# Optimization experiments

Measured on AMD Instinct MI355X. Metric: run time of the kernel, lower is better.

## Reference

```python
import jax, jax.numpy as jnp
import numpy as np

B, K, T, C, F = 2048, 32, 365, 4, 128  # batch, prototypes, steps, bands, feature_size


def conv1d(x, w, b, pad):
    # x: (B, Cin, T), w: (Cout, Cin, Kw)
    y = jax.lax.conv_general_dilated(x, w, (1,), [(pad, pad)],
                                     dimension_numbers=('NCH', 'OIH', 'NCH'))
    return y + b[None, :, None]


def bn_relu(x, gamma, beta):
    # training-mode BatchNorm1d over (batch, time) per channel
    mu = x.mean((0, 2), keepdims=True)
    var = x.var((0, 2), keepdims=True)
    xn = (x - mu) * jax.lax.rsqrt(var + 1e-5)
    return jax.nn.relu(xn * gamma[None, :, None] + beta[None, :, None])


def encoder(x, w1, b1, g1, be1, w2, b2, g2, be2, w3, b3, g3, be3, fc_w, fc_b):
    # FCNBaseline: 3 conv blocks + global average pool + linear
    h = x.transpose(0, 2, 1)                    # (B, C, T)
    h = bn_relu(conv1d(h, w1, b1, 4), g1, be1)  # (B, 128, T+1)
    h = bn_relu(conv1d(h, w2, b2, 2), g2, be2)  # (B, 256, *)
    h = bn_relu(conv1d(h, w3, b3, 1), g3, be3)  # (B, 128, *)
    return h.mean(-1) @ fc_w.T + fc_b           # (B, F)


def setup_inputs() -> dict:
    key = jax.random.key(0)
    ks = jax.random.split(key, 12)
    input_seq = jax.random.normal(ks[0], (B, T, C), jnp.float32)
    label = jax.random.randint(ks[1], (B,), 0, 9)
    mask = (jax.random.uniform(ks[2], (B, T)) > 0.2).astype(jnp.float32)
    prototypes = jax.random.normal(ks[3], (K, T, C), jnp.float32)
    w1 = jax.random.normal(ks[4], (128, C, 8)) * 0.05
    b1 = jnp.zeros((128,)); g1 = jnp.ones((128,)); be1 = jnp.zeros((128,))
    w2 = jax.random.normal(ks[5], (256, 128, 5)) * 0.05
    b2 = jnp.zeros((256,)); g2 = jnp.ones((256,)); be2 = jnp.zeros((256,))
    w3 = jax.random.normal(ks[6], (128, 256, 3)) * 0.05
    b3 = jnp.zeros((128,)); g3 = jnp.ones((128,)); be3 = jnp.zeros((128,))
    fc_w = jax.random.normal(ks[7], (F, 128)) * 0.05
    fc_b = jnp.zeros((F,))
    off_w = jax.random.normal(ks[8], (K * C, F)) * 0.05
    off_b = jnp.zeros((K * C,))
    return dict(input_seq=input_seq, label=label, mask=mask, prototypes=prototypes,
                w1=w1, b1=b1, g1=g1, be1=be1, w2=w2, b2=b2, g2=g2, be2=be2,
                w3=w3, b3=b3, g3=g3, be3=be3, fc_w=fc_w, fc_b=fc_b,
                off_w=off_w, off_b=off_b)


def reference(input_seq, label, mask, prototypes, w1, b1, g1, be1, w2, b2, g2, be2,
              w3, b3, g3, be3, fc_w, fc_b, off_w, off_b):
    # trans_activ=False (TPS warp disabled), offset_activ=True, unsupervised path
    feat = encoder(input_seq, w1, b1, g1, be1, w2, b2, g2, be2, w3, b3, g3, be3, fc_w, fc_b)
    offset = jnp.tanh(feat @ off_w.T + off_b).reshape(-1, K, 1, C)  # (B,K,1,C)
    protos = prototypes[None] + offset                              # (B,K,T,C)
    diff = input_seq[:, None] - protos                              # (B,K,T,C)
    # masked squared-distance reduce: mask (B,T) broadcasts over (K,C)
    distances = jnp.einsum('bktc,bt->bk', diff * diff, mask)        # (B,K)
    indices = jnp.argmin(distances, axis=1)                         # (B,)
    output_seq = jnp.take_along_axis(protos, indices[:, None, None, None], axis=1)[:, 0]
    return output_seq
```

## Files before the change

### kernel.cpp

```cpp
#include <hip/hip_runtime.h>
#include <hip/hip_bf16.h>

#define BB 2048
#define TIN 365
#define TO 366
#define C1 128
#define C2 256
#define C3 128
#define FF 128

typedef __attribute__((ext_vector_type(4))) float f32x4v;
typedef __attribute__((ext_vector_type(8))) short bf16x8;

__device__ inline unsigned short f2bf(float v) {
  unsigned u = __float_as_uint(v);
  unsigned r = (u + 0x7FFF + ((u >> 16) & 1)) >> 16;
  return (unsigned short)r;
}
__device__ inline float bf2f(unsigned short b) {
  return __uint_as_float(((unsigned)b) << 16);
}

__global__ void wtrans_kernel(const float* __restrict__ wsrc, float* __restrict__ wdst,
                              int Cout, int Cin, int Kw) {
// ... 21 lines not shown
    size_t dst = ((((size_t)k * 4 + (i >> 5)) * 16 + (o >> 4)) * 64 +
                  ((i >> 3) & 3) * 16 + (o & 15)) * 8 + (i & 7);
    wh[dst] = (short)hb;
    wl[dst] = (short)lb;
  }
}
__global__ void wprep3_kernel(const float* __restrict__ w3,
                              short* __restrict__ wh, short* __restrict__ wl) {
  int n = 128 * 256 * 3;
  for (int idx = blockIdx.x * 256 + threadIdx.x; idx < n; idx += gridDim.x * 256) {
    int k = idx % 3;
    int rest = idx / 3;
    int i = rest % 256;
    int o = rest / 256;
    float v = w3[idx];
    unsigned short hb = f2bf(v);
    unsigned short lb = f2bf(v - bf2f(hb));
    size_t dst = ((((size_t)k * 8 + (i >> 5)) * 8 + (o >> 4)) * 64 +
                  ((i >> 3) & 3) * 16 + (o & 15)) * 8 + (i & 7);
    wh[dst] = (short)hb;
    wl[dst] = (short)lb;
  }
}

__global__ void bnparam_kernel(const double* __restrict__ sums,
                               const float* __restrict__ gamma,
                               const float* __restrict__ beta, int Cch,
                               float* __restrict__ scale, float* __restrict__ shift) {
  int i = threadIdx.x;
  if (i < Cch) {
    const double N = (double)BB * (double)TO;
    double mean = sums[i] / N;
    double var = sums[Cch + i] / N - mean * mean;
    double sc = (double)gamma[i] / sqrt(var + 1e-5);
    scale[i] = (float)sc;
    shift[i] = (float)((double)beta[i] - mean * sc);
  }
}

__global__ __launch_bounds__(256) void conv1_stats_kernel(
    const float* __restrict__ x, const float* __restrict__ w1,
    const float* __restrict__ b1, double* __restrict__ sums) {
  __shared__ float4 xs[374];
  __shared__ float ws1[4096];
  int tid = threadIdx.x;
  for (int i = tid; i < 4096; i += 256) ws1[i] = w1[i];
  __syncthreads();
  const int o = tid >> 1, half = tid & 1;
  float wr[32];
#pragma unroll
  for (int i = 0; i < 32; ++i) wr[i] = ws1[o * 32 + i];
  const float bo = b1[o];
  float s1 = 0.f, s2 = 0.f;
  for (int b = blockIdx.x * 8; b < blockIdx.x * 8 + 8; ++b) {
    __syncthreads();
    for (int u = tid; u < 374; u += 256) {
      int t_in = u - 4;
      float4 v = make_float4(0.f, 0.f, 0.f, 0.f);
      if (t_in >= 0 && t_in < TIN) v = *(const float4*)(x + ((size_t)b * TIN + t_in) * 4);
      xs[u] = v;
    }
    __syncthreads();
    for (int t = half * 183; t < half * 183 + 183; ++t) {
      float acc = bo;
#pragma unroll
      for (int k = 0; k < 8; ++k) {
        float4 xv = xs[t + k];
        acc = fmaf(wr[k], xv.x, acc);
        acc = fmaf(wr[8 + k], xv.y, acc);
        acc = fmaf(wr[16 + k], xv.z, acc);
        acc = fmaf(wr[24 + k], xv.w, acc);
      }
      s1 += acc; s2 += acc * acc;
    }
  }
  s1 += __shfl_xor(s1, 1);
  s2 += __shfl_xor(s2, 1);
  if (half == 0) {
    atomicAdd(&sums[o], (double)s1);
    atomicAdd(&sums[C1 + o], (double)s2);
  }
}

__global__ __launch_bounds__(256) void conv2_mfma_kernel(
    const float* __restrict__ x, const float* __restrict__ w1g,
    const float* __restrict__ b1, const float* __restrict__ scale1,
    const float* __restrict__ shift1, const short* __restrict__ w2ph,
    const short* __restrict__ w2pl, const float* __restrict__ b2,
    float* __restrict__ p2) {
  __shared__ float ws1[4096];
  __shared__ float4 xwin[76];
  __shared__ __align__(16) short h1h[68 * 72];
  __shared__ __align__(16) short h1l[68 * 72];
  __shared__ float sstat[512];
  const int tid = threadIdx.x;
  const int tt = blockIdx.x, b = blockIdx.y;
  const int tbase = tt * 64;
  const int slice = (b * 6 + tt) & 63;
  const int w = tid >> 6, lane = tid & 63;
  const int q = lane >> 4, l15 = lane & 15;

  for (int i = tid; i < 4096; i += 256) ws1[i] = w1g[i];
  for (int u = tid; u < 76; u += 256) {
    int tx = tbase - 6 + u;
    float4 v = make_float4(0.f, 0.f, 0.f, 0.f);
    if (tx >= 0 && tx < TIN) v = *(const float4*)(x + ((size_t)b * TIN + tx) * 4);
    xwin[u] = v;
  }
  float b2r[4][4];
#pragma unroll
  for (int om = 0; om < 4; ++om)
#pragma unroll
    for (int r = 0; r < 4; ++r) b2r[om][r] = b2[64 * w + om * 16 + q * 4 + r];

  f32x4v acc[4][4];
#pragma unroll
  for (int om = 0; om < 4; ++om)
#pragma unroll
    for (int nt = 0; nt < 4; ++nt) acc[om][nt] = (f32x4v){0.f, 0.f, 0.f, 0.f};

  const int chl = tid >> 2, qt = tid & 3;
  for (int ic2 = 0; ic2 < 2; ++ic2) {
    __syncthreads();
    {
      int ch = ic2 * 64 + chl;
      float sc = scale1[ch], sh = shift1[ch], bo = b1[ch];
      const float* wr = &ws1[ch * 32];
      for (int j = 0; j < 17; ++j) {
        int u = qt * 17 + j;
        int t = tbase - 2 + u;
        float a = bo;
#pragma unroll
        for (int kk = 0; kk < 8; ++kk) {
          float4 xv = xwin[u + kk];
          a = fmaf(wr[kk], xv.x, a);
          a = fmaf(wr[8 + kk], xv.y, a);
          a = fmaf(wr[16 + kk], xv.z, a);
          a = fmaf(wr[24 + kk], xv.w, a);
        }
        float v = (t >= 0 && t < TO) ? fmaxf(fmaf(sc, a, sh), 0.f) : 0.f;
        unsigned short hb = f2bf(v);
        h1h[u * 72 + chl] = (short)hb;
        h1l[u * 72 + chl] = (short)f2bf(v - bf2f(hb));
      }
    }
    __syncthreads();
    for (int k = 0; k < 5; ++k) {
      for (int ic = 0; ic < 2; ++ic) {
        int icg = ic2 * 2 + ic;
        bf16x8 ah[4], al[4];
#pragma unroll
        for (int om = 0; om < 4; ++om) {
          int og = 4 * w + om;
          size_t base = ((((size_t)k * 4 + icg) * 16 + og) * 64 + lane) * 8;
          ah[om] = *(const bf16x8*)(w2ph + base);
          al[om] = *(const bf16x8*)(w2pl + base);
        }
        int ioff = ic * 32 + q * 8;
#pragma unroll
        for (int nt = 0; nt < 4; ++nt) {
          int u = nt * 16 + l15 + k;
          bf16x8 bh = *(const bf16x8*)&h1h[u * 72 + ioff];
          bf16x8 bl = *(const bf16x8*)&h1l[u * 72 + ioff];
#pragma unroll
          for (int om = 0; om < 4; ++om) {
            acc[om][nt] = __builtin_amdgcn_mfma_f32_16x16x32_bf16(ah[om], bh, acc[om][nt], 0, 0, 0);
            acc[om][nt] = __builtin_amdgcn_mfma_f32_16x16x32_bf16(ah[om], bl, acc[om][nt], 0, 0, 0);
            acc[om][nt] = __builtin_amdgcn_mfma_f32_16x16x32_bf16(al[om], bh, acc[om][nt], 0, 0, 0);
          }
        }
      }
    }
  }
  float ts1[16], ts2[16];
#pragma unroll
  for (int i = 0; i < 16; ++i) { ts1[i] = 0.f; ts2[i] = 0.f; }
#pragma unroll
  for (int om = 0; om < 4; ++om)
#pragma unroll
    for (int nt = 0; nt < 4; ++nt) {
      int t = tbase + nt * 16 + l15;
      if (t < TO) {
#pragma unroll
        for (int r = 0; r < 4; ++r) {
          float v = acc[om][nt][r] + b2r[om][r];
          ts1[om * 4 + r] += v;
          ts2[om * 4 + r] += v * v;
        }
      }
    }
#pragma unroll
  for (int i = 0; i < 16; ++i) {
#pragma unroll
    for (int d = 1; d < 16; d <<= 1) {
      ts1[i] += __shfl_xor(ts1[i], d);
      ts2[i] += __shfl_xor(ts2[i], d);
    }
  }
  if (l15 == 0) {
#pragma unroll
    for (int om = 0; om < 4; ++om)
#pragma unroll
      for (int r = 0; r < 4; ++r) {
        int o = 64 * w + om * 16 + q * 4 + r;
        sstat[o] = ts1[om * 4 + r];
        sstat[256 + o] = ts2[om * 4 + r];
      }
  }
  __syncthreads();
  atomicAdd(&p2[(size_t)tid * 64 + slice], sstat[tid]);
  atomicAdd(&p2[((size_t)tid + 256) * 64 + slice], sstat[tid + 256]);
}

template <int EPI>
__global__ __launch_bounds__(256) void fused23_kernel(
    const float* __restrict__ x, const float* __restrict__ w1g,
    const float* __restrict__ b1, const float* __restrict__ scale1,
    const float* __restrict__ shift1, const short* __restrict__ w2ph,
    const short* __restrict__ w2pl, const float* __restrict__ b2,
    const float* __restrict__ scale2, const float* __restrict__ shift2,
    const short* __restrict__ w3ph, const short* __restrict__ w3pl,
    const float* __restrict__ b3, const float* __restrict__ scale3,
    const float* __restrict__ shift3, float* __restrict__ p3,
    float* __restrict__ pooled) {
  __shared__ float4 xwin[80];
  __shared__ __align__(16) short un[34848];
  __shared__ float bn2s[768];
  __shared__ float sstat[256];
  short* h1h = un;
  short* h1l = un + 70 * 72;
  short* h2sh = un;
  short* h2sl = un + 66 * 264;
  const int tid = threadIdx.x;
  const int tt = blockIdx.x, b = blockIdx.y;
  const int tbase = tt * 64;
  const int slice = (b * 6 + tt) & 63;
  const int w = tid >> 6, lane = tid & 63;
  const int q = lane >> 4, l15 = lane & 15;

  for (int u = tid; u < 77; u += 256) {
    int tx = tbase - 7 + u;
    float4 v = make_float4(0.f, 0.f, 0.f, 0.f);
    if (tx >= 0 && tx < TIN) v = *(const float4*)(x + ((size_t)b * TIN + tx) * 4);
    xwin[u] = v;
  }
  bn2s[tid] = b2[tid];
  bn2s[256 + tid] = scale2[tid];
  bn2s[512 + tid] = shift2[tid];

  float b3r[2][4], sc3r[2][4], sh3r[2][4];
#pragma unroll
  for (int om = 0; om < 2; ++om)
#pragma unroll
    for (int r = 0; r < 4; ++r) {
      int o = 32 * w + om * 16 + q * 4 + r;
      b3r[om][r] = b3[o];
      if (EPI == 1) { sc3r[om][r] = scale3[o]; sh3r[om][r] = shift3[o]; }
    }

  f32x4v acc2[4][5];
#pragma unroll
  for (int om = 0; om < 4; ++om)
#pragma unroll
    for (int nt = 0; nt < 5; ++nt) acc2[om][nt] = (f32x4v){0.f, 0.f, 0.f, 0.f};

  const int chl = tid >> 2, qt = tid & 3;
  for (int ic2 = 0; ic2 < 2; ++ic2) {
    int ch = ic2 * 64 + chl;
    float wr[32];
#pragma unroll
    for (int i = 0; i < 32; ++i) wr[i] = w1g[ch * 32 + i];
    float sc = scale1[ch], sh = shift1[ch], bo = b1[ch];
    __syncthreads();
    for (int j = 0; j < 18; ++j) {
      int u1 = qt * 18 + j;
      if (u1 < 70) {
        int t1 = tbase - 3 + u1;
        float a = bo;
#pragma unroll
        for (int kk = 0; kk < 8; ++kk) {
          float4 xv = xwin[u1 + kk];
          a = fmaf(wr[kk], xv.x, a);
          a = fmaf(wr[8 + kk], xv.y, a);
          a = fmaf(wr[16 + kk], xv.z, a);
          a = fmaf(wr[24 + kk], xv.w, a);
        }
        float v = (t1 >= 0 && t1 < TO) ? fmaxf(fmaf(sc, a, sh), 0.f) : 0.f;
        unsigned short hb = f2bf(v);
        h1h[u1 * 72 + chl] = (short)hb;
        h1l[u1 * 72 + chl] = (short)f2bf(v - bf2f(hb));
      }
    }
    __syncthreads();
    for (int k = 0; k < 5; ++k) {
// ... 81 lines not shown
      }
    }
  }
  if (EPI == 0) {
    float ts1[8], ts2[8];
#pragma unroll
    for (int i = 0; i < 8; ++i) { ts1[i] = 0.f; ts2[i] = 0.f; }
#pragma unroll
    for (int om = 0; om < 2; ++om)
#pragma unroll
      for (int nt = 0; nt < 4; ++nt) {
        int t = tbase + nt * 16 + l15;
        if (t < TO) {
#pragma unroll
          for (int r = 0; r < 4; ++r) {
            float v = acc3[om][nt][r] + b3r[om][r];
            ts1[om * 4 + r] += v;
            ts2[om * 4 + r] += v * v;
          }
        }
      }
#pragma unroll
    for (int i = 0; i < 8; ++i) {
#pragma unroll
      for (int d = 1; d < 16; d <<= 1) {
        ts1[i] += __shfl_xor(ts1[i], d);
        ts2[i] += __shfl_xor(ts2[i], d);
      }
    }
    if (l15 == 0) {
#pragma unroll
      for (int om = 0; om < 2; ++om)
#pragma unroll
        for (int r = 0; r < 4; ++r) {
          int o = 32 * w + om * 16 + q * 4 + r;
          sstat[o] = ts1[om * 4 + r];
          sstat[128 + o] = ts2[om * 4 + r];
        }
    }
    __syncthreads();
    atomicAdd(&p3[(size_t)tid * 64 + slice], sstat[tid]);
  } else {
    float ps[8];
#pragma unroll
    for (int i = 0; i < 8; ++i) ps[i] = 0.f;
#pragma unroll
    for (int om = 0; om < 2; ++om)
#pragma unroll
      for (int nt = 0; nt < 4; ++nt) {
        int t = tbase + nt * 16 + l15;
        if (t < TO) {
#pragma unroll
          for (int r = 0; r < 4; ++r) {
            float v = acc3[om][nt][r] + b3r[om][r];
            ps[om * 4 + r] += fmaxf(fmaf(sc3r[om][r], v, sh3r[om][r]), 0.f);
          }
        }
      }
#pragma unroll
    for (int i = 0; i < 8; ++i) {
#pragma unroll
      for (int d = 1; d < 16; d <<= 1) ps[i] += __shfl_xor(ps[i], d);
    }
    if (l15 == 0) {
#pragma unroll
      for (int om = 0; om < 2; ++om)
#pragma unroll
        for (int r = 0; r < 4; ++r) {
          int o = 32 * w + om * 16 + q * 4 + r;
          atomicAdd(&pooled[(size_t)b * 128 + o], ps[om * 4 + r]);
        }
    }
  }
}

__global__ __launch_bounds__(64) void reduce_slices_kernel(
    const float* __restrict__ p, double* __restrict__ sums) {
  int c = blockIdx.x, tid = threadIdx.x;
  double s = (double)p[(size_t)c * 64 + tid];
  for (int d = 32; d > 0; d >>= 1) s += __shfl_down(s, d);
  if (tid == 0) sums[c] = s;
}

__global__ __launch_bounds__(256) void conv12_kernel(
    const float* __restrict__ x, const float* __restrict__ w1g,
    const float* __restrict__ b1, const float* __restrict__ scale1,
    const float* __restrict__ shift1, const float* __restrict__ w2t,
    const float* __restrict__ b2, double* __restrict__ sums2) {
  __shared__ __align__(16) float xs[32][72];
  __shared__ __align__(16) float wsb[32 * 5 * 64];
  __shared__ float4 xwin[80];
  __shared__ float ws1[4096];
  __shared__ float s1s[64], s2s[64];
  const int tid = threadIdx.x;
  const int tbase = blockIdx.x * 64;
  const int obase = blockIdx.y * 64;
  const int bb0 = blockIdx.z * 16;
  for (int i = tid; i < 4096; i += 256) ws1[i] = w1g[i];
  if (tid < 64) { s1s[tid] = 0.f; s2s[tid] = 0.f; }
  const int t0 = (tid & 15) * 4;
  const int o0 = (tid >> 4) * 4;
  const int mch = tid >> 3, mug = tid & 7;
  float b2r[4];
#pragma unroll
  for (int oo = 0; oo < 4; ++oo) b2r[oo] = b2[obase + o0 + oo];
  float ts1[4] = {}, ts2[4] = {};
  for (int b = bb0; b < bb0 + 16; ++b) {
    __syncthreads();
    for (int u = tid; u < 76; u += 256) {
      int tx = tbase - 6 + u;
      float4 v = make_float4(0.f, 0.f, 0.f, 0.f);
      if (tx >= 0 && tx < TIN) v = *(const float4*)(x + ((size_t)b * TIN + tx) * 4);
      xwin[u] = v;
    }
    __syncthreads();
    float acc[4][4] = {};
    for (int ic = 0; ic < C1; ic += 32) {
      {
        int ch = ic + mch;
        float wr[32];
#pragma unroll
        for (int i = 0; i < 32; ++i) wr[i] = ws1[ch * 32 + i];
        float bo = b1[ch], sc = scale1[ch], sh = shift1[ch];
#pragma unroll
        for (int j = 0; j < 9; ++j) {
          int uu = mug * 9 + j;
          if (uu < 68) {
            int v = tbase - 2 + uu;
            float a = bo;
#pragma unroll
            for (int k = 0; k < 8; ++k) {
              float4 xv = xwin[uu + k];
              a = fmaf(wr[k], xv.x, a);
              a = fmaf(wr[8 + k], xv.y, a);
              a = fmaf(wr[16 + k], xv.z, a);
              a = fmaf(wr[24 + k], xv.w, a);
            }
            xs[mch][uu] = (v >= 0 && v < TO) ? fmaxf(fmaf(sc, a, sh), 0.f) : 0.f;
          }
        }
      }
      {
        const float* wsrc = w2t + (size_t)(ic * 5) * C2 + obase;
        for (int idx = tid; idx < 32 * 5 * 64; idx += 256) {
          int o = idx & 63, row = idx >> 6;
          wsb[idx] = wsrc[(size_t)row * C2 + o];
        }
      }
      __syncthreads();
#pragma unroll 4
      for (int ii = 0; ii < 32; ++ii) {
        float xv[8];
#pragma unroll
        for (int d = 0; d < 8; ++d) xv[d] = xs[ii][t0 + d];
#pragma unroll
        for (int k = 0; k < 5; ++k) {
          float4 wv = *(const float4*)&wsb[(ii * 5 + k) * 64 + o0];
#pragma unroll
          for (int tz = 0; tz < 4; ++tz) {
            float xvv = xv[k + tz];
            acc[0][tz] = fmaf(wv.x, xvv, acc[0][tz]);
            acc[1][tz] = fmaf(wv.y, xvv, acc[1][tz]);
            acc[2][tz] = fmaf(wv.z, xvv, acc[2][tz]);
            acc[3][tz] = fmaf(wv.w, xvv, acc[3][tz]);
          }
        }
      }
      __syncthreads();
    }
#pragma unroll
    for (int oo = 0; oo < 4; ++oo) {
#pragma unroll
      for (int tz = 0; tz < 4; ++tz) {
        int t = tbase + t0 + tz;
        if (t < TO) {
          float v = acc[oo][tz] + b2r[oo];
          ts1[oo] += v; ts2[oo] += v * v;
        }
      }
    }
  }
  __syncthreads();
#pragma unroll
  for (int oo = 0; oo < 4; ++oo) {
    atomicAdd(&s1s[o0 + oo], ts1[oo]);
    atomicAdd(&s2s[o0 + oo], ts2[oo]);
  }
  __syncthreads();
  if (tid < 64) {
    atomicAdd(&sums2[obase + tid], (double)s1s[tid]);
    atomicAdd(&sums2[C2 + obase + tid], (double)s2s[tid]);
  }
}

template <int EPI>
__global__ __launch_bounds__(256) void conv23_kernel(
    const float* __restrict__ x, const float* __restrict__ w1g,
    const float* __restrict__ b1, const float* __restrict__ scale1,
    const float* __restrict__ shift1, const float* __restrict__ w2t,
    const float* __restrict__ b2, const float* __restrict__ scale2,
    const float* __restrict__ shift2, const float* __restrict__ w3t,
    const float* __restrict__ b3, const float* __restrict__ scale3,
    const float* __restrict__ shift3, double* __restrict__ sums3,
    float* __restrict__ pooled) {
  __shared__ float4 xwin[80];
  __shared__ float ws1[4096];
  __shared__ float h1buf[128][72];
  __shared__ float h2c[32][68];
  __shared__ float red[128], red2[128];
  const int tid = threadIdx.x;
  const int tbase = blockIdx.x * 64;
  const int bb0 = blockIdx.y * 8;
  for (int i = tid; i < 4096; i += 256) ws1[i] = w1g[i];
  const int t3 = (tid & 15) * 4;
  const int og = tid >> 4;
  float b3r[8], sc3r[8], sh3r[8];
#pragma unroll
  for (int oo = 0; oo < 8; ++oo) {
    int o = og * 8 + oo;
    b3r[oo] = b3[o];
    if (EPI == 1) { sc3r[oo] = scale3[o]; sh3r[oo] = shift3[o]; }
  }
  const int c1ch = tid >> 1, c1half = tid & 1;
  float wr1[32]; float c1b = 0.f, c1sc = 0.f, c1sh = 0.f;
  const int oc2 = tid & 31, ug = tid >> 5;
  const int base2 = ug * 9;
  const int jmax = (66 - base2) < 9 ? (66 - base2) : 9;
  float ts1[8] = {}, ts2[8] = {};
  bool wr1_loaded = false;
  for (int b = bb0; b < bb0 + 8; ++b) {
    __syncthreads();
    for (int u = tid; u < 78; u += 256) {
      int tx = tbase - 7 + u;
      float4 v = make_float4(0.f, 0.f, 0.f, 0.f);
      if (tx >= 0 && tx < TIN) v = *(const float4*)(x + ((size_t)b * TIN + tx) * 4);
      xwin[u] = v;
    }
    __syncthreads();
    if (!wr1_loaded) {
#pragma unroll
      for (int i = 0; i < 32; ++i) wr1[i] = ws1[c1ch * 32 + i];
      c1b = b1[c1ch]; c1sc = scale1[c1ch]; c1sh = shift1[c1ch];
      wr1_loaded = true;
    }
    for (int j = 0; j < 35; ++j) {
      int uu = c1half * 35 + j;
      int v = tbase - 3 + uu;
      float a = c1b;
#pragma unroll
      for (int k = 0; k < 8; ++k) {
        float4 xv = xwin[uu + k];
        a = fmaf(wr1[k], xv.x, a);
        a = fmaf(wr1[8 + k], xv.y, a);
        a = fmaf(wr1[16 + k], xv.z, a);
        a = fmaf(wr1[24 + k], xv.w, a);
      }
      h1buf[c1ch][uu] = (v >= 0 && v < TO) ? fmaxf(fmaf(c1sc, a, c1sh), 0.f) : 0.f;
    }
    float acc3[8][4] = {};
    for (int ocb = 0; ocb < 8; ++ocb) {
      __syncthreads();
      {
        int oc = ocb * 32 + oc2;
        float acc2[9];
#pragma unroll
        for (int j = 0; j < 9; ++j) acc2[j] = 0.f;
        for (int i = 0; i < 128; ++i) {
          const float* wrow = w2t + (size_t)i * 5 * C2 + oc;
          float wk0 = wrow[0], wk1 = wrow[C2], wk2 = wrow[2 * C2],
                wk3 = wrow[3 * C2], wk4 = wrow[4 * C2];
          float w0 = h1buf[i][base2 + 0], w1v = h1buf[i][base2 + 1],
                w2v = h1buf[i][base2 + 2], w3v = h1buf[i][base2 + 3],
                w4v = h1buf[i][base2 + 4];
#pragma unroll
          for (int j = 0; j < 9; ++j) {
            if (j < jmax) {
              float s = wk0 * w0;
              s = fmaf(wk1, w1v, s);
              s = fmaf(wk2, w2v, s);
              s = fmaf(wk3, w3v, s);
              s = fmaf(wk4, w4v, s);
              acc2[j] += s;
              if (j + 1 < jmax) {
                w0 = w1v; w1v = w2v; w2v = w3v; w3v = w4v;
                w4v = h1buf[i][base2 + j + 5];
              }
            }
          }
        }
        float bo2 = b2[oc], sc2v = scale2[oc], sh2v = shift2[oc];
#pragma unroll
        for (int j = 0; j < 9; ++j) {
          if (j < jmax) {
            int uu = base2 + j;
            int u = tbase - 1 + uu;
            float v = acc2[j] + bo2;
            h2c[oc2][uu] = (u >= 0 && u < TO) ? fmaxf(fmaf(sc2v, v, sh2v), 0.f) : 0.f;
          }
        }
      }
      __syncthreads();
      for (int i2 = 0; i2 < 32; ++i2) {
        int i = ocb * 32 + i2;
        float h0 = h2c[i2][t3 + 0], h1v = h2c[i2][t3 + 1], h2v = h2c[i2][t3 + 2],
              h3v = h2c[i2][t3 + 3], h4v = h2c[i2][t3 + 4], h5v = h2c[i2][t3 + 5];
        const float* w3row = w3t + (size_t)i * 3 * C3 + og * 8;
#pragma unroll
        for (int k = 0; k < 3; ++k) {
          float4 wa = *(const float4*)(w3row + k * C3);
          float4 wb = *(const float4*)(w3row + k * C3 + 4);
          float hv0 = (k == 0) ? h0 : ((k == 1) ? h1v : h2v);
          float hv1 = (k == 0) ? h1v : ((k == 1) ? h2v : h3v);
          float hv2 = (k == 0) ? h2v : ((k == 1) ? h3v : h4v);
          float hv3 = (k == 0) ? h3v : ((k == 1) ? h4v : h5v);
          float hv[4] = {hv0, hv1, hv2, hv3};
#pragma unroll
          for (int tz = 0; tz < 4; ++tz) {
            acc3[0][tz] = fmaf(wa.x, hv[tz], acc3[0][tz]);
            acc3[1][tz] = fmaf(wa.y, hv[tz], acc3[1][tz]);
            acc3[2][tz] = fmaf(wa.z, hv[tz], acc3[2][tz]);
            acc3[3][tz] = fmaf(wa.w, hv[tz], acc3[3][tz]);
            acc3[4][tz] = fmaf(wb.x, hv[tz], acc3[4][tz]);
            acc3[5][tz] = fmaf(wb.y, hv[tz], acc3[5][tz]);
            acc3[6][tz] = fmaf(wb.z, hv[tz], acc3[6][tz]);
            acc3[7][tz] = fmaf(wb.w, hv[tz], acc3[7][tz]);
          }
        }
      }
    }
    if (EPI == 0) {
#pragma unroll
      for (int oo = 0; oo < 8; ++oo) {
#pragma unroll
        for (int tz = 0; tz < 4; ++tz) {
          int t = tbase + t3 + tz;
          if (t < TO) {
            float v = acc3[oo][tz] + b3r[oo];
            ts1[oo] += v; ts2[oo] += v * v;
          }
        }
      }
    } else {
      __syncthreads();
      if (tid < 128) red[tid] = 0.f;
      __syncthreads();
#pragma unroll
      for (int oo = 0; oo < 8; ++oo) {
        float s = 0.f;
#pragma unroll
        for (int tz = 0; tz < 4; ++tz) {
          int t = tbase + t3 + tz;
          if (t < TO)
            s += fmaxf(fmaf(sc3r[oo], acc3[oo][tz] + b3r[oo], sh3r[oo]), 0.f);
        }
        atomicAdd(&red[og * 8 + oo], s);
      }
      __syncthreads();
      if (tid < 128) atomicAdd(&pooled[(size_t)b * C3 + tid], red[tid]);
    }
  }
  if (EPI == 0) {
    __syncthreads();
    if (tid < 128) { red[tid] = 0.f; red2[tid] = 0.f; }
    __syncthreads();
#pragma unroll
    for (int oo = 0; oo < 8; ++oo) {
      atomicAdd(&red[og * 8 + oo], ts1[oo]);
      atomicAdd(&red2[og * 8 + oo], ts2[oo]);
    }
    __syncthreads();
    if (tid < 128) {
      atomicAdd(&sums3[tid], (double)red[tid]);
      atomicAdd(&sums3[C3 + tid], (double)red2[tid]);
    }
  }
}

__global__ __launch_bounds__(128) void head2_kernel(
    const float* __restrict__ pooled, const float* __restrict__ fc_w,
    const float* __restrict__ fc_b, const float* __restrict__ off_w,
    const float* __restrict__ off_b, float* __restrict__ offs) {
  int b = blockIdx.x, tid = threadIdx.x;
  __shared__ float pl[128], feat[128];
  pl[tid] = pooled[(size_t)b * C3 + tid] * (1.0f / 366.0f);
  __syncthreads();
  {
    const float* wr = fc_w + tid * FF;
    float a = fc_b[tid];
    for (int i = 0; i < 128; ++i) a = fmaf(pl[i], wr[i], a);
    feat[tid] = a;
  }
  __syncthreads();
  {
    const float* wr = off_w + tid * FF;
    float z = off_b[tid];
    for (int i = 0; i < 128; ++i) z = fmaf(feat[i], wr[i], z);
    offs[(size_t)b * 128 + tid] = tanhf(z);
  }
}

__global__ __launch_bounds__(256) void dist_kernel(
    const float* __restrict__ x, const float* __restrict__ mask,
    const float* __restrict__ protos, const float* __restrict__ offs,
    float* __restrict__ out) {
  int b = blockIdx.x, tid = threadIdx.x;
  __shared__ float ofl[128];
  __shared__ double dred[256];
  __shared__ int ksel;
  if (tid < 128) ofl[tid] = offs[(size_t)b * 128 + tid];
  __syncthreads();
  int k = tid & 31, tg = tid >> 5;
  float o0 = ofl[k * 4 + 0], o1 = ofl[k * 4 + 1], o2 = ofl[k * 4 + 2], o3 = ofl[k * 4 + 3];
  double acc = 0.0;
  for (int t = tg; t < TIN; t += 8) {
    float4 xv = *(const float4*)(x + ((size_t)b * TIN + t) * 4);
    float4 pv = *(const float4*)(protos + ((size_t)k * TIN + t) * 4);
    float m = mask[(size_t)b * TIN + t];
    float d0 = xv.x - pv.x - o0;
    float d1 = xv.y - pv.y - o1;
    float d2 = xv.z - pv.z - o2;
    float d3 = xv.w - pv.w - o3;
    acc += (double)(m * (d0 * d0 + d1 * d1 + d2 * d2 + d3 * d3));
  }
  dred[tid] = acc;
  __syncthreads();
  if (tid < 32) {
    double s = 0.0;
    for (int g = 0; g < 8; ++g) s += dred[g * 32 + tid];
    dred[tid] = s;
  }
  __syncthreads();
  if (tid == 0) {
    double best = dred[0]; int bi = 0;
    for (int kk = 1; kk < 32; ++kk)
      if (dred[kk] < best) { best = dred[kk]; bi = kk; }
    ksel = bi;
  }
  __syncthreads();
  int km = ksel;
  const float* psrc = protos + (size_t)km * TIN * 4;
  float* dst = out + (size_t)b * TIN * 4;
  for (int u = tid; u < TIN * 4; u += 256)
    dst[u] = psrc[u] + ofl[km * 4 + (u & 3)];
}

extern "C" void kernel_launch(void* const* d_in, const int* in_sizes, int n_in,
                              void* d_out, int out_size, void* d_ws, size_t ws_size,
                              hipStream_t stream) {
  const float* x      = (const float*)d_in[0];
  const float* mask   = (const float*)d_in[2];
  const float* protos = (const float*)d_in[3];
  const float* w1 = (const float*)d_in[4];
  const float* b1 = (const float*)d_in[5];
  const float* g1 = (const float*)d_in[6];
  const float* be1 = (const float*)d_in[7];
  const float* w2 = (const float*)d_in[8];
  const float* b2 = (const float*)d_in[9];
  const float* g2 = (const float*)d_in[10];
  const float* be2 = (const float*)d_in[11];
  const float* w3 = (const float*)d_in[12];
  const float* b3 = (const float*)d_in[13];
  const float* g3 = (const float*)d_in[14];
  const float* be3 = (const float*)d_in[15];
  const float* fc_w = (const float*)d_in[16];
  const float* fc_b = (const float*)d_in[17];
  const float* off_w = (const float*)d_in[18];
  const float* off_b = (const float*)d_in[19];
  float* out = (float*)d_out;
  (void)in_sizes; (void)n_in; (void)out_size;

  char* wsp = (char*)d_ws;
  size_t off = 0;
  auto alloc = [&](size_t bytes) { void* p = wsp + off; off += (bytes + 255) & ~(size_t)255; return p; };
  float* w2t   = (float*)alloc((size_t)C1 * 5 * C2 * 4);
  float* w3t   = (float*)alloc((size_t)C2 * 3 * C3 * 4);
  float* bnp   = (float*)alloc(1024 * 4);
  float* offs  = (float*)alloc((size_t)BB * 128 * 4);
  size_t zero_beg = off;
  double* sums  = (double*)alloc(1024 * 8);
  float* pooled = (float*)alloc((size_t)BB * C3 * 4);
  float* p2     = (float*)alloc((size_t)512 * 64 * 4);
  float* p3     = (float*)alloc((size_t)256 * 64 * 4);
  size_t zero_end = off;
  short* w2ph = (short*)alloc((size_t)256 * 128 * 5 * 2);
  short* w2pl = (short*)alloc((size_t)256 * 128 * 5 * 2);
  short* w3ph = (short*)alloc((size_t)128 * 256 * 3 * 2);
  short* w3pl = (short*)alloc((size_t)128 * 256 * 3 * 2);
  size_t small_end = off;
  const bool mfma_ok = ws_size >= small_end;

  double* sums1 = sums;
  double* sums2 = sums + 256;
  double* sums3 = sums + 768;
  float* scale1 = bnp;        float* shift1 = bnp + 128;
  float* scale2 = bnp + 256;  float* shift2 = bnp + 512;
  float* scale3 = bnp + 768;  float* shift3 = bnp + 896;

  hipMemsetAsync(wsp + zero_beg, 0, zero_end - zero_beg, stream);

  conv1_stats_kernel<<<256, 256, 0, stream>>>(x, w1, b1, sums1);
  bnparam_kernel<<<1, 256, 0, stream>>>(sums1, g1, be1, C1, scale1, shift1);

  if (mfma_ok) {
    wprep2_kernel<<<256, 256, 0, stream>>>(w2, w2ph, w2pl);
    wprep3_kernel<<<128, 256, 0, stream>>>(w3, w3ph, w3pl);

    conv2_mfma_kernel<<<dim3(6, BB), 256, 0, stream>>>(
        x, w1, b1, scale1, shift1, w2ph, w2pl, b2, p2);
    reduce_slices_kernel<<<512, 64, 0, stream>>>(p2, sums2);
    bnparam_kernel<<<1, 256, 0, stream>>>(sums2, g2, be2, C2, scale2, shift2);

    fused23_kernel<0><<<dim3(6, BB), 256, 0, stream>>>(
        x, w1, b1, scale1, shift1, w2ph, w2pl, b2, scale2, shift2,
        w3ph, w3pl, b3, scale3, shift3, p3, pooled);
    reduce_slices_kernel<<<256, 64, 0, stream>>>(p3, sums3);
    bnparam_kernel<<<1, 256, 0, stream>>>(sums3, g3, be3, C3, scale3, shift3);

    fused23_kernel<1><<<dim3(6, BB), 256, 0, stream>>>(
        x, w1, b1, scale1, shift1, w2ph, w2pl, b2, scale2, shift2,
        w3ph, w3pl, b3, scale3, shift3, p3, pooled);
  } else {
    wtrans_kernel<<<256, 256, 0, stream>>>(w2, w2t, C2, C1, 5);
    wtrans_kernel<<<96, 256, 0, stream>>>(w3, w3t, C3, C2, 3);
    conv12_kernel<<<dim3(6, 4, 128), 256, 0, stream>>>(
        x, w1, b1, scale1, shift1, w2t, b2, sums2);
    bnparam_kernel<<<1, 256, 0, stream>>>(sums2, g2, be2, C2, scale2, shift2);
    conv23_kernel<0><<<dim3(6, 256), 256, 0, stream>>>(
        x, w1, b1, scale1, shift1, w2t, b2, scale2, shift2, w3t, b3, scale3, shift3,
        sums3, pooled);
    bnparam_kernel<<<1, 256, 0, stream>>>(sums3, g3, be3, C3, scale3, shift3);
    conv23_kernel<1><<<dim3(6, 256), 256, 0, stream>>>(
        x, w1, b1, scale1, shift1, w2t, b2, scale2, shift2, w3t, b3, scale3, shift3,
        sums3, pooled);
  }

  head2_kernel<<<BB, 128, 0, stream>>>(pooled, fc_w, fc_b, off_w, off_b, offs);
  dist_kernel<<<BB, 256, 0, stream>>>(x, mask, protos, offs, out);
}
```

Baseline: 3.879 ms.

## Materialize conv2 output in workspace instead of recomputing conv1+conv2 per pass

The conv2 MFMA pass now also stores its pre-BN output to a large global buffer. Two new conv3-only passes read that buffer, apply BN2+ReLU, split to bf16 hi/lo and run the conv3 MFMA. The old fused kernels recomputed conv1 and conv2 in both conv3 passes. This trades heavy recomputation for roughly 770MB of writes plus two reads of it. The new path only runs when the workspace is large enough, and the scalar fallback kernels are removed.

```diff
diff --git a/kernel.cpp b/kernel.cpp
--- a/kernel.cpp
+++ b/kernel.cpp
@@ -127,12 +127,13 @@
   }
 }
 
+template <bool STORE>
 __global__ __launch_bounds__(256) void conv2_mfma_kernel(
     const float* __restrict__ x, const float* __restrict__ w1g,
     const float* __restrict__ b1, const float* __restrict__ scale1,
     const float* __restrict__ shift1, const short* __restrict__ w2ph,
     const short* __restrict__ w2pl, const float* __restrict__ b2,
-    float* __restrict__ p2) {
+    float* __restrict__ p2, float* __restrict__ h2g) {
   __shared__ float ws1[4096];
   __shared__ float4 xwin[76];
   __shared__ __align__(16) short h1h[68 * 72];
@@ -231,6 +232,10 @@
           float v = acc[om][nt][r] + b2r[om][r];
           ts1[om * 4 + r] += v;
           ts2[om * 4 + r] += v * v;
+          if (STORE) {
+            int o = 64 * w + om * 16 + q * 4 + r;
+            h2g[((size_t)b * 256 + o) * 368 + t] = v;
+          }
         }
       }
     }
@@ -255,6 +260,156 @@
   __syncthreads();
   atomicAdd(&p2[(size_t)tid * 64 + slice], sstat[tid]);
   atomicAdd(&p2[((size_t)tid + 256) * 64 + slice], sstat[tid + 256]);
+}
+
+template <int EPI>
+__global__ __launch_bounds__(256) void conv3_pass_kernel(
+    const float* __restrict__ h2g, const float* __restrict__ scale2,
+    const float* __restrict__ shift2, const short* __restrict__ w3ph,
+    const short* __restrict__ w3pl, const float* __restrict__ b3,
+    const float* __restrict__ scale3, const float* __restrict__ shift3,
+    float* __restrict__ p3, float* __restrict__ pooled) {
+  __shared__ __align__(16) short h2sh[66 * 264];
+  __shared__ __align__(16) short h2sl[66 * 264];
+  __shared__ float sstat[256];
+  const int tid = threadIdx.x;
+  const int tt = blockIdx.x, b = blockIdx.y;
+  const int tbase = tt * 64;
+  const int slice = (b * 6 + tt) & 63;
+  const int w = tid >> 6, lane = tid & 63;
+  const int q = lane >> 4, l15 = lane & 15;
+
+  float b3r[2][4], sc3r[2][4], sh3r[2][4];
+#pragma unroll
+  for (int om = 0; om < 2; ++om)
+#pragma unroll
+    for (int r = 0; r < 4; ++r) {
+      int o = 32 * w + om * 16 + q * 4 + r;
+      b3r[om][r] = b3[o];
+      if (EPI == 1) { sc3r[om][r] = scale3[o]; sh3r[om][r] = shift3[o]; }
+    }
+
+  for (int cc = 0; cc < 64; ++cc) {
+    int ch = w * 64 + cc;
+    float sc = scale2[ch], sh = shift2[ch];
+    const float* src = h2g + ((size_t)b * 256 + ch) * 368;
+    int t2 = tbase - 1 + lane;
+    float v = 0.f;
+    if (t2 >= 0 && t2 < TO) v = fmaxf(fmaf(sc, src[t2], sh), 0.f);
+    unsigned short hb = f2bf(v);
+    h2sh[lane * 264 + ch] = (short)hb;
+    h2sl[lane * 264 + ch] = (short)f2bf(v - bf2f(hb));
+    if (lane < 2) {
+      int u2 = 64 + lane;
+      int t2b = tbase - 1 + u2;
+      float vb = 0.f;
+      if (t2b >= 0 && t2b < TO) vb = fmaxf(fmaf(sc, src[t2b], sh), 0.f);
+      unsigned short hbb = f2bf(vb);
+      h2sh[u2 * 264 + ch] = (short)hbb;
+      h2sl[u2 * 264 + ch] = (short)f2bf(vb - bf2f(hbb));
+    }
+  }
+  __syncthreads();
+  f32x4v acc3[2][4];
+#pragma unroll
+  for (int om = 0; om < 2; ++om)
+#pragma unroll
+    for (int nt = 0; nt < 4; ++nt) acc3[om][nt] = (f32x4v){0.f, 0.f, 0.f, 0.f};
+  for (int k = 0; k < 3; ++k) {
+    for (int icg = 0; icg < 8; ++icg) {
+      bf16x8 a3h[2], a3l[2];
+#pragma unroll
+      for (int om = 0; om < 2; ++om) {
+        int og = 2 * w + om;
+        size_t base = ((((size_t)k * 8 + icg) * 8 + og) * 64 + lane) * 8;
+        a3h[om] = *(const bf16x8*)(w3ph + base);
+        a3l[om] = *(const bf16x8*)(w3pl + base);
+      }
+      int ioff = icg * 32 + q * 8;
+#pragma unroll
+      for (int nt = 0; nt < 4; ++nt) {
+        int u = nt * 16 + l15 + k;
+        bf16x8 bh = *(const bf16x8*)&h2sh[u * 264 + ioff];
+        bf16x8 bl = *(const bf16x8*)&h2sl[u * 264 + ioff];
+#pragma unroll
+        for (int om = 0; om < 2; ++om) {
+          acc3[om][nt] = __builtin_amdgcn_mfma_f32_16x16x32_bf16(a3h[om], bh, acc3[om][nt], 0, 0, 0);
+          acc3[om][nt] = __builtin_amdgcn_mfma_f32_16x16x32_bf16(a3l[om], bh, acc3[om][nt], 0, 0, 0);
+          acc3[om][nt] = __builtin_amdgcn_mfma_f32_16x16x32_bf16(a3h[om], bl, acc3[om][nt], 0, 0, 0);
+        }
+      }
+    }
+  }
+  if (EPI == 0) {
+    float ts1[8], ts2[8];
+#pragma unroll
+    for (int i = 0; i < 8; ++i) { ts1[i] = 0.f; ts2[i] = 0.f; }
+#pragma unroll
+    for (int om = 0; om < 2; ++om)
+#pragma unroll
+      for (int nt = 0; nt < 4; ++nt) {
+        int t = tbase + nt * 16 + l15;
+        if (t < TO) {
+#pragma unroll
+          for (int r = 0; r < 4; ++r) {
+            float v = acc3[om][nt][r] + b3r[om][r];
+            ts1[om * 4 + r] += v;
+            ts2[om * 4 + r] += v * v;
+          }
+        }
+      }
+#pragma unroll
+    for (int i = 0; i < 8; ++i) {
+#pragma unroll
+      for (int d = 1; d < 16; d <<= 1) {
+        ts1[i] += __shfl_xor(ts1[i], d);
+        ts2[i] += __shfl_xor(ts2[i], d);
+      }
+    }
+    if (l15 == 0) {
+#pragma unroll
+      for (int om = 0; om < 2; ++om)
+#pragma unroll
+        for (int r = 0; r < 4; ++r) {
+          int o = 32 * w + om * 16 + q * 4 + r;
+          sstat[o] = ts1[om * 4 + r];
+          sstat[128 + o] = ts2[om * 4 + r];
+        }
+    }
+    __syncthreads();
+    atomicAdd(&p3[(size_t)tid * 64 + slice], sstat[tid]);
+  } else {
+    float ps[8];
+#pragma unroll
+    for (int i = 0; i < 8; ++i) ps[i] = 0.f;
+#pragma unroll
+    for (int om = 0; om < 2; ++om)
+#pragma unroll
+      for (int nt = 0; nt < 4; ++nt) {
+        int t = tbase + nt * 16 + l15;
+        if (t < TO) {
+#pragma unroll
+          for (int r = 0; r < 4; ++r) {
+            float v = acc3[om][nt][r] + b3r[om][r];
+            ps[om * 4 + r] += fmaxf(fmaf(sc3r[om][r], v, sh3r[om][r]), 0.f);
+          }
+        }
+      }
+#pragma unroll
+    for (int i = 0; i < 8; ++i) {
+#pragma unroll
+      for (int d = 1; d < 16; d <<= 1) ps[i] += __shfl_xor(ps[i], d);
+    }
+    if (l15 == 0) {
+#pragma unroll
+      for (int om = 0; om < 2; ++om)
+#pragma unroll
+        for (int r = 0; r < 4; ++r) {
+          int o = 32 * w + om * 16 + q * 4 + r;
+          atomicAdd(&pooled[(size_t)b * 128 + o], ps[om * 4 + r]);
+        }
+    }
+  }
 }
 
 template <int EPI>
@@ -502,300 +657,6 @@
   if (tid == 0) sums[c] = s;
 }
 
-__global__ __launch_bounds__(256) void conv12_kernel(
-    const float* __restrict__ x, const float* __restrict__ w1g,
-    const float* __restrict__ b1, const float* __restrict__ scale1,
-    const float* __restrict__ shift1, const float* __restrict__ w2t,
-    const float* __restrict__ b2, double* __restrict__ sums2) {
-  __shared__ __align__(16) float xs[32][72];
-  __shared__ __align__(16) float wsb[32 * 5 * 64];
-  __shared__ float4 xwin[80];
-  __shared__ float ws1[4096];
-  __shared__ float s1s[64], s2s[64];
-  const int tid = threadIdx.x;
-  const int tbase = blockIdx.x * 64;
-  const int obase = blockIdx.y * 64;
-  const int bb0 = blockIdx.z * 16;
-  for (int i = tid; i < 4096; i += 256) ws1[i] = w1g[i];
-  if (tid < 64) { s1s[tid] = 0.f; s2s[tid] = 0.f; }
-  const int t0 = (tid & 15) * 4;
-  const int o0 = (tid >> 4) * 4;
-  const int mch = tid >> 3, mug = tid & 7;
-  float b2r[4];
-#pragma unroll
-  for (int oo = 0; oo < 4; ++oo) b2r[oo] = b2[obase + o0 + oo];
-  float ts1[4] = {}, ts2[4] = {};
-  for (int b = bb0; b < bb0 + 16; ++b) {
-    __syncthreads();
-    for (int u = tid; u < 76; u += 256) {
-      int tx = tbase - 6 + u;
-      float4 v = make_float4(0.f, 0.f, 0.f, 0.f);
-      if (tx >= 0 && tx < TIN) v = *(const float4*)(x + ((size_t)b * TIN + tx) * 4);
-      xwin[u] = v;
-    }
-    __syncthreads();
-    float acc[4][4] = {};
-    for (int ic = 0; ic < C1; ic += 32) {
-      {
-        int ch = ic + mch;
-        float wr[32];
-#pragma unroll
-        for (int i = 0; i < 32; ++i) wr[i] = ws1[ch * 32 + i];
-        float bo = b1[ch], sc = scale1[ch], sh = shift1[ch];
-#pragma unroll
-        for (int j = 0; j < 9; ++j) {
-          int uu = mug * 9 + j;
-          if (uu < 68) {
-            int v = tbase - 2 + uu;
-            float a = bo;
-#pragma unroll
-            for (int k = 0; k < 8; ++k) {
-              float4 xv = xwin[uu + k];
-              a = fmaf(wr[k], xv.x, a);
-              a = fmaf(wr[8 + k], xv.y, a);
-              a = fmaf(wr[16 + k], xv.z, a);
-              a = fmaf(wr[24 + k], xv.w, a);
-            }
-            xs[mch][uu] = (v >= 0 && v < TO) ? fmaxf(fmaf(sc, a, sh), 0.f) : 0.f;
-          }
-        }
-      }
-      {
-        const float* wsrc = w2t + (size_t)(ic * 5) * C2 + obase;
-        for (int idx = tid; idx < 32 * 5 * 64; idx += 256) {
-          int o = idx & 63, row = idx >> 6;
-          wsb[idx] = wsrc[(size_t)row * C2 + o];
-        }
-      }
-      __syncthreads();
-#pragma unroll 4
-      for (int ii = 0; ii < 32; ++ii) {
-        float xv[8];
-#pragma unroll
-        for (int d = 0; d < 8; ++d) xv[d] = xs[ii][t0 + d];
-#pragma unroll
-        for (int k = 0; k < 5; ++k) {
-          float4 wv = *(const float4*)&wsb[(ii * 5 + k) * 64 + o0];
-#pragma unroll
-          for (int tz = 0; tz < 4; ++tz) {
-            float xvv = xv[k + tz];
-            acc[0][tz] = fmaf(wv.x, xvv, acc[0][tz]);
-            acc[1][tz] = fmaf(wv.y, xvv, acc[1][tz]);
-            acc[2][tz] = fmaf(wv.z, xvv, acc[2][tz]);
-            acc[3][tz] = fmaf(wv.w, xvv, acc[3][tz]);
-          }
-        }
-      }
-      __syncthreads();
-    }
-#pragma unroll
-    for (int oo = 0; oo < 4; ++oo) {
-#pragma unroll
-      for (int tz = 0; tz < 4; ++tz) {
-        int t = tbase + t0 + tz;
-        if (t < TO) {
-          float v = acc[oo][tz] + b2r[oo];
-          ts1[oo] += v; ts2[oo] += v * v;
-        }
-      }
-    }
-  }
-  __syncthreads();
-#pragma unroll
-  for (int oo = 0; oo < 4; ++oo) {
-    atomicAdd(&s1s[o0 + oo], ts1[oo]);
-    atomicAdd(&s2s[o0 + oo], ts2[oo]);
-  }
-  __syncthreads();
-  if (tid < 64) {
-    atomicAdd(&sums2[obase + tid], (double)s1s[tid]);
-    atomicAdd(&sums2[C2 + obase + tid], (double)s2s[tid]);
-  }
-}
-
-template <int EPI>
-__global__ __launch_bounds__(256) void conv23_kernel(
-    const float* __restrict__ x, const float* __restrict__ w1g,
-    const float* __restrict__ b1, const float* __restrict__ scale1,
-    const float* __restrict__ shift1, const float* __restrict__ w2t,
-    const float* __restrict__ b2, const float* __restrict__ scale2,
-    const float* __restrict__ shift2, const float* __restrict__ w3t,
-    const float* __restrict__ b3, const float* __restrict__ scale3,
-    const float* __restrict__ shift3, double* __restrict__ sums3,
-    float* __restrict__ pooled) {
-  __shared__ float4 xwin[80];
-  __shared__ float ws1[4096];
-  __shared__ float h1buf[128][72];
-  __shared__ float h2c[32][68];
-  __shared__ float red[128], red2[128];
-  const int tid = threadIdx.x;
-  const int tbase = blockIdx.x * 64;
-  const int bb0 = blockIdx.y * 8;
-  for (int i = tid; i < 4096; i += 256) ws1[i] = w1g[i];
-  const int t3 = (tid & 15) * 4;
-  const int og = tid >> 4;
-  float b3r[8], sc3r[8], sh3r[8];
-#pragma unroll
-  for (int oo = 0; oo < 8; ++oo) {
-    int o = og * 8 + oo;
-    b3r[oo] = b3[o];
-    if (EPI == 1) { sc3r[oo] = scale3[o]; sh3r[oo] = shift3[o]; }
-  }
-  const int c1ch = tid >> 1, c1half = tid & 1;
-  float wr1[32]; float c1b = 0.f, c1sc = 0.f, c1sh = 0.f;
-  const int oc2 = tid & 31, ug = tid >> 5;
-  const int base2 = ug * 9;
-  const int jmax = (66 - base2) < 9 ? (66 - base2) : 9;
-  float ts1[8] = {}, ts2[8] = {};
-  bool wr1_loaded = false;
-  for (int b = bb0; b < bb0 + 8; ++b) {
-    __syncthreads();
-    for (int u = tid; u < 78; u += 256) {
-      int tx = tbase - 7 + u;
-      float4 v = make_float4(0.f, 0.f, 0.f, 0.f);
-      if (tx >= 0 && tx < TIN) v = *(const float4*)(x + ((size_t)b * TIN + tx) * 4);
-      xwin[u] = v;
-    }
-    __syncthreads();
-    if (!wr1_loaded) {
-#pragma unroll
-      for (int i = 0; i < 32; ++i) wr1[i] = ws1[c1ch * 32 + i];
-      c1b = b1[c1ch]; c1sc = scale1[c1ch]; c1sh = shift1[c1ch];
-      wr1_loaded = true;
-    }
-    for (int j = 0; j < 35; ++j) {
-      int uu = c1half * 35 + j;
-      int v = tbase - 3 + uu;
-      float a = c1b;
-#pragma unroll
-      for (int k = 0; k < 8; ++k) {
-        float4 xv = xwin[uu + k];
-        a = fmaf(wr1[k], xv.x, a);
-        a = fmaf(wr1[8 + k], xv.y, a);
-        a = fmaf(wr1[16 + k], xv.z, a);
-        a = fmaf(wr1[24 + k], xv.w, a);
-      }
-      h1buf[c1ch][uu] = (v >= 0 && v < TO) ? fmaxf(fmaf(c1sc, a, c1sh), 0.f) : 0.f;
-    }
-    float acc3[8][4] = {};
-    for (int ocb = 0; ocb < 8; ++ocb) {
-      __syncthreads();
-      {
-        int oc = ocb * 32 + oc2;
-        float acc2[9];
-#pragma unroll
-        for (int j = 0; j < 9; ++j) acc2[j] = 0.f;
-        for (int i = 0; i < 128; ++i) {
-          const float* wrow = w2t + (size_t)i * 5 * C2 + oc;
-          float wk0 = wrow[0], wk1 = wrow[C2], wk2 = wrow[2 * C2],
-                wk3 = wrow[3 * C2], wk4 = wrow[4 * C2];
-          float w0 = h1buf[i][base2 + 0], w1v = h1buf[i][base2 + 1],
-                w2v = h1buf[i][base2 + 2], w3v = h1buf[i][base2 + 3],
-                w4v = h1buf[i][base2 + 4];
-#pragma unroll
-          for (int j = 0; j < 9; ++j) {
-            if (j < jmax) {
-              float s = wk0 * w0;
-              s = fmaf(wk1, w1v, s);
-              s = fmaf(wk2, w2v, s);
-              s = fmaf(wk3, w3v, s);
-              s = fmaf(wk4, w4v, s);
-              acc2[j] += s;
-              if (j + 1 < jmax) {
-                w0 = w1v; w1v = w2v; w2v = w3v; w3v = w4v;
-                w4v = h1buf[i][base2 + j + 5];
-              }
-            }
-          }
-        }
-        float bo2 = b2[oc], sc2v = scale2[oc], sh2v = shift2[oc];
-#pragma unroll
-        for (int j = 0; j < 9; ++j) {
-          if (j < jmax) {
-            int uu = base2 + j;
-            int u = tbase - 1 + uu;
-            float v = acc2[j] + bo2;
-            h2c[oc2][uu] = (u >= 0 && u < TO) ? fmaxf(fmaf(sc2v, v, sh2v), 0.f) : 0.f;
-          }
-        }
-      }
-      __syncthreads();
-      for (int i2 = 0; i2 < 32; ++i2) {
-        int i = ocb * 32 + i2;
-        float h0 = h2c[i2][t3 + 0], h1v = h2c[i2][t3 + 1], h2v = h2c[i2][t3 + 2],
-              h3v = h2c[i2][t3 + 3], h4v = h2c[i2][t3 + 4], h5v = h2c[i2][t3 + 5];
-        const float* w3row = w3t + (size_t)i * 3 * C3 + og * 8;
-#pragma unroll
-        for (int k = 0; k < 3; ++k) {
-          float4 wa = *(const float4*)(w3row + k * C3);
-          float4 wb = *(const float4*)(w3row + k * C3 + 4);
-          float hv0 = (k == 0) ? h0 : ((k == 1) ? h1v : h2v);
-          float hv1 = (k == 0) ? h1v : ((k == 1) ? h2v : h3v);
-          float hv2 = (k == 0) ? h2v : ((k == 1) ? h3v : h4v);
-          float hv3 = (k == 0) ? h3v : ((k == 1) ? h4v : h5v);
-          float hv[4] = {hv0, hv1, hv2, hv3};
-#pragma unroll
-          for (int tz = 0; tz < 4; ++tz) {
-            acc3[0][tz] = fmaf(wa.x, hv[tz], acc3[0][tz]);
-            acc3[1][tz] = fmaf(wa.y, hv[tz], acc3[1][tz]);
-            acc3[2][tz] = fmaf(wa.z, hv[tz], acc3[2][tz]);
-            acc3[3][tz] = fmaf(wa.w, hv[tz], acc3[3][tz]);
-            acc3[4][tz] = fmaf(wb.x, hv[tz], acc3[4][tz]);
-            acc3[5][tz] = fmaf(wb.y, hv[tz], acc3[5][tz]);
-            acc3[6][tz] = fmaf(wb.z, hv[tz], acc3[6][tz]);
-            acc3[7][tz] = fmaf(wb.w, hv[tz], acc3[7][tz]);
-          }
-        }
-      }
-    }
-    if (EPI == 0) {
-#pragma unroll
-      for (int oo = 0; oo < 8; ++oo) {
-#pragma unroll
-        for (int tz = 0; tz < 4; ++tz) {
-          int t = tbase + t3 + tz;
-          if (t < TO) {
-            float v = acc3[oo][tz] + b3r[oo];
-            ts1[oo] += v; ts2[oo] += v * v;
-          }
-        }
-      }
-    } else {
-      __syncthreads();
-      if (tid < 128) red[tid] = 0.f;
-      __syncthreads();
-#pragma unroll
-      for (int oo = 0; oo < 8; ++oo) {
-        float s = 0.f;
-#pragma unroll
-        for (int tz = 0; tz < 4; ++tz) {
-          int t = tbase + t3 + tz;
-          if (t < TO)
-            s += fmaxf(fmaf(sc3r[oo], acc3[oo][tz] + b3r[oo], sh3r[oo]), 0.f);
-        }
-        atomicAdd(&red[og * 8 + oo], s);
-      }
-      __syncthreads();
-      if (tid < 128) atomicAdd(&pooled[(size_t)b * C3 + tid], red[tid]);
-    }
-  }
-  if (EPI == 0) {
-    __syncthreads();
-    if (tid < 128) { red[tid] = 0.f; red2[tid] = 0.f; }
-    __syncthreads();
-#pragma unroll
-    for (int oo = 0; oo < 8; ++oo) {
-      atomicAdd(&red[og * 8 + oo], ts1[oo]);
-      atomicAdd(&red2[og * 8 + oo], ts2[oo]);
-    }
-    __syncthreads();
-    if (tid < 128) {
-      atomicAdd(&sums3[tid], (double)red[tid]);
-      atomicAdd(&sums3[C3 + tid], (double)red2[tid]);
-    }
-  }
-}
-
 __global__ __launch_bounds__(128) void head2_kernel(
     const float* __restrict__ pooled, const float* __restrict__ fc_w,
     const float* __restrict__ fc_b, const float* __restrict__ off_w,
@@ -892,8 +753,6 @@
   char* wsp = (char*)d_ws;
   size_t off = 0;
   auto alloc = [&](size_t bytes) { void* p = wsp + off; off += (bytes + 255) & ~(size_t)255; return p; };
-  float* w2t   = (float*)alloc((size_t)C1 * 5 * C2 * 4);
-  float* w3t   = (float*)alloc((size_t)C2 * 3 * C3 * 4);
   float* bnp   = (float*)alloc(1024 * 4);
   float* offs  = (float*)alloc((size_t)BB * 128 * 4);
   size_t zero_beg = off;
@@ -908,6 +767,9 @@
   short* w3pl = (short*)alloc((size_t)128 * 256 * 3 * 2);
   size_t small_end = off;
   const bool mfma_ok = ws_size >= small_end;
+  const size_t h2_bytes = (size_t)BB * 256 * 368 * 4;
+  float* h2 = (float*)(wsp + small_end);
+  const bool h2_ok = ws_size >= small_end + h2_bytes;
 
   double* sums1 = sums;
   double* sums2 = sums + 256;
@@ -925,33 +787,31 @@
     wprep2_kernel<<<256, 256, 0, stream>>>(w2, w2ph, w2pl);
     wprep3_kernel<<<128, 256, 0, stream>>>(w3, w3ph, w3pl);
 
-    conv2_mfma_kernel<<<dim3(6, BB), 256, 0, stream>>>(
-        x, w1, b1, scale1, shift1, w2ph, w2pl, b2, p2);
-    reduce_slices_kernel<<<512, 64, 0, stream>>>(p2, sums2);
-    bnparam_kernel<<<1, 256, 0, stream>>>(sums2, g2, be2, C2, scale2, shift2);
-
-    fused23_kernel<0><<<dim3(6, BB), 256, 0, stream>>>(
-        x, w1, b1, scale1, shift1, w2ph, w2pl, b2, scale2, shift2,
-        w3ph, w3pl, b3, scale3, shift3, p3, pooled);
-    reduce_slices_kernel<<<256, 64, 0, stream>>>(p3, sums3);
-    bnparam_kernel<<<1, 256, 0, stream>>>(sums3, g3, be3, C3, scale3, shift3);
-
-    fused23_kernel<1><<<dim3(6, BB), 256, 0, stream>>>(
-        x, w1, b1, scale1, shift1, w2ph, w2pl, b2, scale2, shift2,
-        w3ph, w3pl, b3, scale3, shift3, p3, pooled);
-  } else {
-    wtrans_kernel<<<256, 256, 0, stream>>>(w2, w2t, C2, C1, 5);
-    wtrans_kernel<<<96, 256, 0, stream>>>(w3, w3t, C3, C2, 3);
-    conv12_kernel<<<dim3(6, 4, 128), 256, 0, stream>>>(
-        x, w1, b1, scale1, shift1, w2t, b2, sums2);
-    bnparam_kernel<<<1, 256, 0, stream>>>(sums2, g2, be2, C2, scale2, shift2);
-    conv23_kernel<0><<<dim3(6, 256), 256, 0, stream>>>(
-        x, w1, b1, scale1, shift1, w2t, b2, scale2, shift2, w3t, b3, scale3, shift3,
-        sums3, pooled);
-    bnparam_kernel<<<1, 256, 0, stream>>>(sums3, g3, be3, C3, scale3, shift3);
-    conv23_kernel<1><<<dim3(6, 256), 256, 0, stream>>>(
-        x, w1, b1, scale1, shift1, w2t, b2, scale2, shift2, w3t, b3, scale3, shift3,
-        sums3, pooled);
+    if (h2_ok) {
+      conv2_mfma_kernel<true><<<dim3(6, BB), 256, 0, stream>>>(
+          x, w1, b1, scale1, shift1, w2ph, w2pl, b2, p2, h2);
+      reduce_slices_kernel<<<512, 64, 0, stream>>>(p2, sums2);
+      bnparam_kernel<<<1, 256, 0, stream>>>(sums2, g2, be2, C2, scale2, shift2);
+      conv3_pass_kernel<0><<<dim3(6, BB), 256, 0, stream>>>(
+          h2, scale2, shift2, w3ph, w3pl, b3, scale3, shift3, p3, pooled);
+      reduce_slices_kernel<<<256, 64, 0, stream>>>(p3, sums3);
+      bnparam_kernel<<<1, 256, 0, stream>>>(sums3, g3, be3, C3, scale3, shift3);
+      conv3_pass_kernel<1><<<dim3(6, BB), 256, 0, stream>>>(
+          h2, scale2, shift2, w3ph, w3pl, b3, scale3, shift3, p3, pooled);
+    } else {
+      conv2_mfma_kernel<false><<<dim3(6, BB), 256, 0, stream>>>(
+          x, w1, b1, scale1, shift1, w2ph, w2pl, b2, p2, h2);
+      reduce_slices_kernel<<<512, 64, 0, stream>>>(p2, sums2);
+      bnparam_kernel<<<1, 256, 0, stream>>>(sums2, g2, be2, C2, scale2, shift2);
+      fused23_kernel<0><<<dim3(6, BB), 256, 0, stream>>>(
+          x, w1, b1, scale1, shift1, w2ph, w2pl, b2, scale2, shift2,
+          w3ph, w3pl, b3, scale3, shift3, p3, pooled);
+      reduce_slices_kernel<<<256, 64, 0, stream>>>(p3, sums3);
+      bnparam_kernel<<<1, 256, 0, stream>>>(sums3, g3, be3, C3, scale3, shift3);
+      fused23_kernel<1><<<dim3(6, BB), 256, 0, stream>>>(
+          x, w1, b1, scale1, shift1, w2ph, w2pl, b2, scale2, shift2,
+          w3ph, w3pl, b3, scale3, shift3, p3, pooled);
+    }
   }
 
   head2_kernel<<<BB, 128, 0, stream>>>(pooled, fc_w, fc_b, off_w, off_b, offs);
```

Result: no change. 3.914 ms (+0.9%).
